# Optimization experiments

Hardware: AMD Instinct MI355X
Metric: run time of the kernel (lower is better)

Reference implementation:

```python
import jax, jax.numpy as jnp
import numpy as np

B, T, C, H, S = 4, 2048, 1024, 16, 64
LN_EPS = 1e-5
WKV_EPS = 1e-6
K_CLAMP = 30.0


def _ln(x, g, b):
    m = jnp.mean(x, axis=-1, keepdims=True)
    v = jnp.var(x, axis=-1, keepdims=True)
    return (x - m) * jax.lax.rsqrt(v + LN_EPS) * g + b


def _wkv(k, v, time_decay, time_first):
    # k, v: [B,T,H,S]; recurrence in fp32 over time
    decay = jnp.exp(-jnp.exp(time_decay.astype(jnp.float32)))  # [H,S]
    tf = jnp.exp(time_first.astype(jnp.float32))               # [H,S]
    kt = jnp.moveaxis(k, 1, 0).astype(jnp.float32)  # [T,B,H,S]
    vt = jnp.moveaxis(v, 1, 0).astype(jnp.float32)
    # t == 0 special case: state seeded with time_first factor
    w0 = jnp.exp(jnp.minimum(kt[0], K_CLAMP))
    num0 = tf * w0 * vt[0]
    den0 = tf * w0

    def step(carry, xs):
        num, den = carry
        kk, vv = xs
        w = jnp.exp(jnp.minimum(kk, K_CLAMP))
        num = decay * num + w * vv
        den = decay * den + w
        return (num, den), num / (den + WKV_EPS)

    (_, _), rest = jax.lax.scan(step, (num0, den0), (kt[1:], vt[1:]))
    out = jnp.concatenate([(num0 / (den0 + WKV_EPS))[None], rest], axis=0)  # [T,B,H,S]
    return jnp.moveaxis(out, 0, 1)  # [B,T,H,S]


def setup_inputs() -> dict:
    key = jax.random.key(0)
    ks = jax.random.split(key, 8)
    sc = 1.0 / np.sqrt(C)
    sc4 = 1.0 / np.sqrt(4 * C)
    return {
        "x": jax.random.normal(ks[0], (B, T, C), jnp.float32),
        "time_decay": jnp.full((H, S), -5.0, jnp.float32),
        "time_first": jnp.zeros((H, S), jnp.float32),
        "Wk": jax.random.normal(ks[1], (C, C), jnp.float32) * sc,
        "Wv": jax.random.normal(ks[2], (C, C), jnp.float32) * sc,
        "Wr": jax.random.normal(ks[3], (C, C), jnp.float32) * sc,
        "Wo": jax.random.normal(ks[4], (C, C), jnp.float32) * sc,
        "Wffk": jax.random.normal(ks[5], (4 * C, C), jnp.float32) * sc,
        "Wffv": jax.random.normal(ks[6], (C, 4 * C), jnp.float32) * sc4,
        "ln1_g": jnp.ones((C,), jnp.float32),
        "ln1_b": jnp.zeros((C,), jnp.float32),
        "ln2_g": jnp.ones((C,), jnp.float32),
        "ln2_b": jnp.zeros((C,), jnp.float32),
    }


def reference(x, time_decay, time_first, Wk, Wv, Wr, Wo, Wffk, Wffv, ln1_g, ln1_b, ln2_g, ln2_b):
    b, t, c = x.shape
    h, s = time_decay.shape
    xl = _ln(x, ln1_g, ln1_b)
    k = (xl @ Wk.T).reshape(b, t, h, s)
    v = (xl @ Wv.T).reshape(b, t, h, s)
    r = (xl @ Wr.T).reshape(b, t, h, s)
    wkv = _wkv(k, v, time_decay, time_first).astype(x.dtype)
    rwkv = (jax.nn.sigmoid(r) * wkv).reshape(b, t, c)
    x = x + rwkv @ Wo.T
    xl2 = _ln(x, ln2_g, ln2_b)
    ffn = (jax.nn.relu(xl2 @ Wffk.T) ** 2) @ Wffv.T
    return x + ffn
```

## Files before the change

kernel.cpp:

```cpp
#include <hip/hip_runtime.h>
#include <cstdint>
#include <cstddef>

#define TT 2048
#define CC 1024
#define HH 16
#define SS 64
#define MROWS 8192
#define KVRN 3072
#define NCH 32
#define LCH 64

using short8 = __attribute__((ext_vector_type(8))) short;
using f32x4  = __attribute__((ext_vector_type(4))) float;

__device__ __forceinline__ float b2f(unsigned short u) {
  union { unsigned int i; float f; } c; c.i = ((unsigned int)u) << 16; return c.f;
}
__device__ __forceinline__ unsigned short f2b(float f) {
  union { float f; unsigned int i; } c; c.f = f;
  unsigned int r = c.i + 0x7fffu + ((c.i >> 16) & 1u);
  return (unsigned short)(r >> 16);
}

typedef const __attribute__((address_space(1))) unsigned int* gas_ptr;
typedef __attribute__((address_space(3))) unsigned int* las_ptr;
__device__ __forceinline__ void gl_lds16(const unsigned short* g, unsigned short* l) {
  __builtin_amdgcn_global_load_lds((gas_ptr)g, (las_ptr)l, 16, 0, 0);
}

__global__ __launch_bounds__(256) void cvt_ln_kernel(const float* __restrict__ Wk,
                                                     const float* __restrict__ Wv,
                                                     const float* __restrict__ Wr,
                                                     const float* __restrict__ Wo,
                                                     const float* __restrict__ Wffk,
                                                     const float* __restrict__ Wffv,
                                                     unsigned short* __restrict__ dst,
                                                     const float* __restrict__ x,
                                                     const float* __restrict__ g,
                                                     const float* __restrict__ bta,
                                                     unsigned short* __restrict__ xlo) {
  const size_t M1 = 1048576;
  const int tid = threadIdx.x;
  if (blockIdx.x < 12288) {
    size_t i = ((size_t)blockIdx.x * 256 + tid) * 4;
    const float* src; size_t off;
    if      (i <  1 * M1) { src = Wk;   off = 0;      }
    else if (i <  2 * M1) { src = Wv;   off = 1 * M1; }
    else if (i <  3 * M1) { src = Wr;   off = 2 * M1; }
    else if (i <  4 * M1) { src = Wo;   off = 3 * M1; }
    else if (i <  8 * M1) { src = Wffk; off = 4 * M1; }
    else                  { src = Wffv; off = 8 * M1; }
    float4 v = *(const float4*)(src + (i - off));
    *(ushort4*)(dst + i) = make_ushort4(f2b(v.x), f2b(v.y), f2b(v.z), f2b(v.w));
    return;
  }
  const int row = blockIdx.x - 12288;
  const float* xr = x + (size_t)row * CC;
  float4 v = *(const float4*)(xr + tid * 4);
  float s  = v.x + v.y + v.z + v.w;
  float ss = v.x * v.x + v.y * v.y + v.z * v.z + v.w * v.w;
#pragma unroll
  for (int off = 32; off > 0; off >>= 1) {
    s  += __shfl_xor(s, off, 64);
    ss += __shfl_xor(ss, off, 64);
  }
  __shared__ float ls[4], lss[4];
  if ((tid & 63) == 0) { ls[tid >> 6] = s; lss[tid >> 6] = ss; }
  __syncthreads();
  s  = ls[0] + ls[1] + ls[2] + ls[3];
  ss = lss[0] + lss[1] + lss[2] + lss[3];
  const float mean = s * (1.0f / CC);
  const float var  = ss * (1.0f / CC) - mean * mean;
  const float rstd = rsqrtf(var + 1e-5f);
  float4 gv = *(const float4*)(g + tid * 4);
  float4 bv = *(const float4*)(bta + tid * 4);
  ushort4 o = make_ushort4(f2b((v.x - mean) * rstd * gv.x + bv.x),
                           f2b((v.y - mean) * rstd * gv.y + bv.y),
                           f2b((v.z - mean) * rstd * gv.z + bv.z),
                           f2b((v.w - mean) * rstd * gv.w + bv.w));
  *(ushort4*)(xlo + (size_t)row * CC + tid * 4) = o;
}

__global__ __launch_bounds__(256) void ln_kernel(const float* __restrict__ x,
                                                 const float* __restrict__ g,
                                                 const float* __restrict__ bta,
                                                 unsigned short* __restrict__ out,
                                                 float* __restrict__ outc) {
  const int row = blockIdx.x;
  const int tid = threadIdx.x;
  const float* xr = x + (size_t)row * CC;
  float4 v = *(const float4*)(xr + tid * 4);
  *(float4*)(outc + (size_t)row * CC + tid * 4) = v;
  float s  = v.x + v.y + v.z + v.w;
  float ss = v.x * v.x + v.y * v.y + v.z * v.z + v.w * v.w;
#pragma unroll
  for (int off = 32; off > 0; off >>= 1) {
    s  += __shfl_xor(s, off, 64);
    ss += __shfl_xor(ss, off, 64);
  }
  __shared__ float ls[4], lss[4];
  if ((tid & 63) == 0) { ls[tid >> 6] = s; lss[tid >> 6] = ss; }
  __syncthreads();
  s  = ls[0] + ls[1] + ls[2] + ls[3];
  ss = lss[0] + lss[1] + lss[2] + lss[3];
  const float mean = s * (1.0f / CC);
  const float var  = ss * (1.0f / CC) - mean * mean;
  const float rstd = rsqrtf(var + 1e-5f);
  float4 gv = *(const float4*)(g + tid * 4);
  float4 bv = *(const float4*)(bta + tid * 4);
  ushort4 o = make_ushort4(f2b((v.x - mean) * rstd * gv.x + bv.x),
                           f2b((v.y - mean) * rstd * gv.y + bv.y),
                           f2b((v.z - mean) * rstd * gv.z + bv.z),
                           f2b((v.w - mean) * rstd * gv.w + bv.w));
  *(ushort4*)(out + (size_t)row * CC + tid * 4) = o;
}

__global__ __launch_bounds__(64) void wkv_local(const unsigned short* __restrict__ kvr,
                                                const float* __restrict__ td,
                                                const float* __restrict__ tfp,
                                                float* __restrict__ scratch) {
  const int blk = blockIdx.x;
  const int bh = blk >> 5, c = blk & (NCH - 1);
  const int b = bh >> 4, h = bh & 15;
  const int s = threadIdx.x;
  const int ch = h * SS + s;
  const float e = __expf(td[ch]);
  const float d = __expf(-e);
  const float tfir = __expf(tfp[ch]);
  size_t idx = ((size_t)b * TT + (size_t)c * LCH) * KVRN + ch;
  float num = 0.f, den = 0.f;
  for (int i = 0; i < LCH; ++i) {
    float w = __expf(fminf(b2f(kvr[idx]), 30.f));
    if (c == 0 && i == 0) w *= tfir;
    float vv = b2f(kvr[idx + 1024]);
    num = d * num + w * vv;
    den = d * den + w;
    idx += KVRN;
  }
  float* o = scratch + ((size_t)bh * NCH + c) * 128;
  o[s] = num; o[64 + s] = den;
}

__global__ __launch_bounds__(64) void wkv_emit(const unsigned short* __restrict__ kvr,
                                               const float* __restrict__ td,
                                               const float* __restrict__ tfp,
                                               const float* __restrict__ scratch,
                                               unsigned short* __restrict__ rwkv) {
  const int blk = blockIdx.x;
  const int bh = blk >> 5, c = blk & (NCH - 1);
  const int b = bh >> 4, h = bh & 15;
  const int s = threadIdx.x;
  const int ch = h * SS + s;
  const float e = __expf(td[ch]);
  const float d = __expf(-e);
  const float Dc = __expf(-e * (float)LCH);
  const float tfir = __expf(tfp[ch]);
  float num = 0.f, den = 0.f;
  const float* sc = scratch + (size_t)bh * NCH * 128;
  for (int cc = 0; cc < c; ++cc) {
    num = Dc * num + sc[cc * 128 + s];
    den = Dc * den + sc[cc * 128 + 64 + s];
  }
  size_t idx = ((size_t)b * TT + (size_t)c * LCH) * KVRN + ch;
  size_t odx = ((size_t)b * TT + (size_t)c * LCH) * CC + ch;
  for (int i = 0; i < LCH; ++i) {
    float w = __expf(fminf(b2f(kvr[idx]), 30.f));
    if (c == 0 && i == 0) w *= tfir;
    float vv = b2f(kvr[idx + 1024]);
    num = d * num + w * vv;
    den = d * den + w;
    float o = num / (den + 1e-6f);
    float rr = b2f(kvr[idx + 2048]);
    float sg = 1.0f / (1.0f + __expf(-rr));
    rwkv[odx] = f2b(sg * o);
    idx += KVRN;
    odx += CC;
  }
}

#define GBAR do { __builtin_amdgcn_sched_barrier(0); __builtin_amdgcn_s_barrier(); \
                  __builtin_amdgcn_sched_barrier(0); } while (0)
#define WAIT_LGKM0 do { __builtin_amdgcn_s_waitcnt(0xC07F); \
                        __builtin_amdgcn_sched_barrier(0); } while (0)
#define WAIT_VM8   do { __builtin_amdgcn_sched_barrier(0); \
                        __builtin_amdgcn_s_waitcnt(0x0F78); \
                        __builtin_amdgcn_sched_barrier(0); } while (0)

template <int EP>
__global__ __launch_bounds__(512, 2) void gemm256(const unsigned short* __restrict__ A,
                                                  const unsigned short* __restrict__ Bw,
                                                  void* __restrict__ outv,
                                                  const float* __restrict__ res,
                                                  int N, int Kfull, int Kloop) {
  __shared__ __align__(16) unsigned short As[2][2][256][32];
  __shared__ __align__(16) unsigned short Bs[2][2][256][32];
  const int tid = threadIdx.x;

  const int nbn = N >> 8;
  const int per_grp = nbn << 4;
  const int bid = blockIdx.x;
  const int grp = bid / per_grp;
  const int rem = bid - grp * per_grp;
  const int bm = (grp << 4) + (rem & 15);
  const int bn = rem >> 4;
  const int koffb = blockIdx.y * Kloop;
  const int nt = Kloop >> 6;

  const int r0  = tid >> 2;
  const int qsl = ((tid & 3) ^ (r0 & 3)) << 3;
  const unsigned short* gA0 = A  + (size_t)(bm * 256 + r0) * Kfull + koffb + qsl;
  const unsigned short* gA1 = gA0 + (size_t)128 * Kfull;
  const unsigned short* gB0 = Bw + (size_t)(bn * 256 + r0) * Kfull + koffb + qsl;
  const unsigned short* gB1 = gB0 + (size_t)128 * Kfull;
  const int ldsoff = tid * 8;

  auto stA = [&](int bb, int kk, int ko) {
    unsigned short* d = &As[bb][kk][0][0];
    gl_lds16(gA0 + ko, d + ldsoff);
    gl_lds16(gA1 + ko, d + ldsoff + 4096);
  };
  auto stB = [&](int bb, int kk, int ko) {
    unsigned short* d = &Bs[bb][kk][0][0];
    gl_lds16(gB0 + ko, d + ldsoff);
    gl_lds16(gB1 + ko, d + ldsoff + 4096);
  };

  const int lane = tid & 63, w = tid >> 6;
  const int wr = w >> 2, wn = w & 3;
  const int r16 = lane & 15, q = lane >> 4;
  const int qx = (q ^ (r16 & 3)) << 3;
  const unsigned short* fA = &As[0][0][0][0] + (wr * 128 + r16) * 32 + qx;
  const unsigned short* fB = &Bs[0][0][0][0] + (wn * 64  + r16) * 32 + qx;

  f32x4 acc[8][4] = {};
  short8 af[4], bf_[4];

  stA(0, 0, 0);  stB(0, 0, 0);
  stA(0, 1, 32); stB(0, 1, 32);
  stA(1, 0, 64); stB(1, 0, 64);
  WAIT_VM8;
  GBAR;

  int b = 0;
  for (int t = 0; t < nt; ++t, b ^= 1) {
    const unsigned short* fAb = fA + b * 16384;
    const unsigned short* fBb = fB + b * 16384;
    const int t1 = (t + 1 < nt) ? t + 1 : nt - 1;
    const int t2 = (t + 2 < nt) ? t + 2 : nt - 1;
    const int ko1 = (t1 << 6) + 32;
    const int ko2 = (t2 << 6);

#pragma unroll
    for (int i = 0; i < 4; ++i) af[i]  = *(const short8*)(fAb + i * 512);
#pragma unroll
    for (int i = 0; i < 4; ++i) bf_[i] = *(const short8*)(fBb + i * 512);
    stA(b ^ 1, 1, ko1);
    GBAR;
    WAIT_LGKM0;
    __builtin_amdgcn_s_setprio(1);
#pragma unroll
    for (int mi = 0; mi < 4; ++mi)
#pragma unroll
      for (int ni = 0; ni < 4; ++ni)
        acc[mi][ni] = __builtin_amdgcn_mfma_f32_16x16x32_bf16(af[mi], bf_[ni], acc[mi][ni], 0, 0, 0);
    __builtin_amdgcn_s_setprio(0);
    GBAR;

#pragma unroll
    for (int i = 0; i < 4; ++i) af[i] = *(const short8*)(fAb + (4 + i) * 512);
    stB(b ^ 1, 1, ko1);
    WAIT_VM8;
    GBAR;
    WAIT_LGKM0;
    __builtin_amdgcn_s_setprio(1);
#pragma unroll
    for (int mi = 0; mi < 4; ++mi)
#pragma unroll
      for (int ni = 0; ni < 4; ++ni)
        acc[4 + mi][ni] = __builtin_amdgcn_mfma_f32_16x16x32_bf16(af[mi], bf_[ni], acc[4 + mi][ni], 0, 0, 0);
    __builtin_amdgcn_s_setprio(0);
    GBAR;

#pragma unroll
    for (int i = 0; i < 4; ++i) af[i]  = *(const short8*)(fAb + 8192 + i * 512);
#pragma unroll
    for (int i = 0; i < 4; ++i) bf_[i] = *(const short8*)(fBb + 8192 + i * 512);
    stA(b, 0, ko2);
    GBAR;
    WAIT_LGKM0;
    __builtin_amdgcn_s_setprio(1);
#pragma unroll
    for (int mi = 0; mi < 4; ++mi)
#pragma unroll
      for (int ni = 0; ni < 4; ++ni)
        acc[mi][ni] = __builtin_amdgcn_mfma_f32_16x16x32_bf16(af[mi], bf_[ni], acc[mi][ni], 0, 0, 0);
    __builtin_amdgcn_s_setprio(0);
    GBAR;

#pragma unroll
    for (int i = 0; i < 4; ++i) af[i] = *(const short8*)(fAb + 8192 + (4 + i) * 512);
    stB(b, 0, ko2);
    WAIT_VM8;
    GBAR;
    WAIT_LGKM0;
    __builtin_amdgcn_s_setprio(1);
#pragma unroll
    for (int mi = 0; mi < 4; ++mi)
#pragma unroll
      for (int ni = 0; ni < 4; ++ni)
        acc[4 + mi][ni] = __builtin_amdgcn_mfma_f32_16x16x32_bf16(af[mi], bf_[ni], acc[4 + mi][ni], 0, 0, 0);
    __builtin_amdgcn_s_setprio(0);
    GBAR;
  }

  __builtin_amdgcn_s_waitcnt(0x0070);

#pragma unroll
  for (int mi = 0; mi < 8; ++mi) {
#pragma unroll
    for (int r = 0; r < 4; ++r) {
      const int grow = bm * 256 + wr * 128 + mi * 16 + q * 4 + r;
#pragma unroll
      for (int ni = 0; ni < 4; ++ni) {
        const int gcol = bn * 256 + wn * 64 + ni * 16 + r16;
        const size_t idx = (size_t)grow * N + gcol;
        float vv = acc[mi][ni][r];
        if (EP == 2) {
          ((float*)outv)[idx] = res[idx] + vv;
        } else if (EP == 3) {
          unsafeAtomicAdd((float*)outv + idx, vv);
        } else {
          if (EP == 1) { vv = fmaxf(vv, 0.0f); vv = vv * vv; }
          ((unsigned short*)outv)[idx] = f2b(vv);
        }
      }
    }
  }
}

extern "C" void kernel_launch(void* const* d_in, const int* in_sizes, int n_in,
                              void* d_out, int out_size, void* d_ws, size_t ws_size,
                              hipStream_t stream) {
  const float* x    = (const float*)d_in[0];
  const float* td   = (const float*)d_in[1];
  const float* tf   = (const float*)d_in[2];
  const float* Wk   = (const float*)d_in[3];
  const float* Wv   = (const float*)d_in[4];
  const float* Wr   = (const float*)d_in[5];
  const float* Wo   = (const float*)d_in[6];
  const float* Wffk = (const float*)d_in[7];
  const float* Wffv = (const float*)d_in[8];
  const float* g1   = (const float*)d_in[9];
  const float* b1   = (const float*)d_in[10];
  const float* g2   = (const float*)d_in[11];
  const float* b2   = (const float*)d_in[12];
  float* out = (float*)d_out;

  char* ws = (char*)d_ws;
  const size_t MB = 1024ull * 1024ull;
  unsigned short* WB    = (unsigned short*)ws;
  unsigned short* WkvrB = WB;
  unsigned short* WoB   = WB + 3 * 1048576;
  unsigned short* WfkB  = WB + 4 * 1048576;
  unsigned short* WfvB  = WB + 8 * 1048576;
  unsigned short* xl    = (unsigned short*)(ws + 24 * MB);
  unsigned short* kvr   = (unsigned short*)(ws + 40 * MB);
  float*          x2    = (float*)(ws + 88 * MB);
  unsigned short* hb    = (unsigned short*)(ws + 120 * MB);
  float*          wkvS  = (float*)(ws + 184 * MB);
  unsigned short* rwkv  = xl;
  unsigned short* xl2   = kvr;

  cvt_ln_kernel<<<12288 + MROWS, 256, 0, stream>>>(Wk, Wv, Wr, Wo, Wffk, Wffv, WB,
                                                   x, g1, b1, xl);

  gemm256<0><<<dim3((KVRN / 256) * (MROWS / 256), 1), 512, 0, stream>>>(
      xl, WkvrB, kvr, nullptr, KVRN, 1024, 1024);

  wkv_local<<<64 * NCH, 64, 0, stream>>>(kvr, td, tf, wkvS);
  wkv_emit<<<64 * NCH, 64, 0, stream>>>(kvr, td, tf, wkvS, rwkv);

  gemm256<2><<<dim3((CC / 256) * (MROWS / 256), 1), 512, 0, stream>>>(
      rwkv, WoB, x2, x, CC, 1024, 1024);

  ln_kernel<<<MROWS, 256, 0, stream>>>(x2, g2, b2, xl2, out);

  gemm256<1><<<dim3((4096 / 256) * (MROWS / 256), 1), 512, 0, stream>>>(
      xl2, WfkB, hb, nullptr, 4096, 1024, 1024);

  gemm256<3><<<dim3((CC / 256) * (MROWS / 256), 2), 512, 0, stream>>>(
      hb, WfvB, out, nullptr, CC, 4096, 2048);
}
```

Baseline: 485.2 us.

## Restructure GEMM into 4-stage single-barrier pipeline and split-K the output projection

```diff
diff --git a/kernel.cpp b/kernel.cpp
--- a/kernel.cpp
+++ b/kernel.cpp
@@ -39,7 +39,8 @@
                                                      const float* __restrict__ x,
                                                      const float* __restrict__ g,
                                                      const float* __restrict__ bta,
-                                                     unsigned short* __restrict__ xlo) {
+                                                     unsigned short* __restrict__ xlo,
+                                                     float* __restrict__ x2o) {
   const size_t M1 = 1048576;
   const int tid = threadIdx.x;
   if (blockIdx.x < 12288) {
@@ -58,6 +59,7 @@
   const int row = blockIdx.x - 12288;
   const float* xr = x + (size_t)row * CC;
   float4 v = *(const float4*)(xr + tid * 4);
+  *(float4*)(x2o + (size_t)row * CC + tid * 4) = v;
   float s  = v.x + v.y + v.z + v.w;
   float ss = v.x * v.x + v.y * v.y + v.z * v.z + v.w * v.w;
 #pragma unroll
@@ -179,7 +181,7 @@
   }
 }
 
-#define GBAR do { __builtin_amdgcn_sched_barrier(0); __builtin_amdgcn_s_barrier(); \
+#define GBAR do { __builtin_amdgcn_sched_barrier(0); asm volatile("s_barrier"); \
                   __builtin_amdgcn_sched_barrier(0); } while (0)
 #define WAIT_LGKM0 do { __builtin_amdgcn_s_waitcnt(0xC07F); \
                         __builtin_amdgcn_sched_barrier(0); } while (0)
@@ -193,8 +195,8 @@
                                                   void* __restrict__ outv,
                                                   const float* __restrict__ res,
                                                   int N, int Kfull, int Kloop) {
-  __shared__ __align__(16) unsigned short As[2][2][256][32];
-  __shared__ __align__(16) unsigned short Bs[2][2][256][32];
+  __shared__ __align__(16) unsigned short As[4][256][32];
+  __shared__ __align__(16) unsigned short Bs[4][256][32];
   const int tid = threadIdx.x;
 
   const int nbn = N >> 8;
@@ -205,113 +207,61 @@
   const int bm = (grp << 4) + (rem & 15);
   const int bn = rem >> 4;
   const int koffb = blockIdx.y * Kloop;
-  const int nt = Kloop >> 6;
+  const int nt = Kloop >> 5;
 
   const int r0  = tid >> 2;
-  const int qsl = ((tid & 3) ^ (r0 & 3)) << 3;
+  const int qsl = ((tid & 3) ^ ((tid >> 3) & 3)) << 3;
   const unsigned short* gA0 = A  + (size_t)(bm * 256 + r0) * Kfull + koffb + qsl;
   const unsigned short* gA1 = gA0 + (size_t)128 * Kfull;
   const unsigned short* gB0 = Bw + (size_t)(bn * 256 + r0) * Kfull + koffb + qsl;
   const unsigned short* gB1 = gB0 + (size_t)128 * Kfull;
   const int ldsoff = tid * 8;
 
-  auto stA = [&](int bb, int kk, int ko) {
-    unsigned short* d = &As[bb][kk][0][0];
-    gl_lds16(gA0 + ko, d + ldsoff);
-    gl_lds16(gA1 + ko, d + ldsoff + 4096);
-  };
-  auto stB = [&](int bb, int kk, int ko) {
-    unsigned short* d = &Bs[bb][kk][0][0];
-    gl_lds16(gB0 + ko, d + ldsoff);
-    gl_lds16(gB1 + ko, d + ldsoff + 4096);
+  auto stage = [&](int bb, int ko) {
+    unsigned short* da = &As[bb][0][0];
+    unsigned short* db = &Bs[bb][0][0];
+    gl_lds16(gA0 + ko, da + ldsoff);
+    gl_lds16(gA1 + ko, da + ldsoff + 4096);
+    gl_lds16(gB0 + ko, db + ldsoff);
+    gl_lds16(gB1 + ko, db + ldsoff + 4096);
   };
 
   const int lane = tid & 63, w = tid >> 6;
   const int wr = w >> 2, wn = w & 3;
   const int r16 = lane & 15, q = lane >> 4;
-  const int qx = (q ^ (r16 & 3)) << 3;
-  const unsigned short* fA = &As[0][0][0][0] + (wr * 128 + r16) * 32 + qx;
-  const unsigned short* fB = &Bs[0][0][0][0] + (wn * 64  + r16) * 32 + qx;
+  const int qx = (q ^ ((r16 >> 1) & 3)) << 3;
+  const unsigned short* fA = &As[0][0][0] + (wr * 128 + r16) * 32 + qx;
+  const unsigned short* fB = &Bs[0][0][0] + (wn * 64  + r16) * 32 + qx;
 
   f32x4 acc[8][4] = {};
-  short8 af[4], bf_[4];
-
-  stA(0, 0, 0);  stB(0, 0, 0);
-  stA(0, 1, 32); stB(0, 1, 32);
-  stA(1, 0, 64); stB(1, 0, 64);
+  short8 af[8], bf_[4];
+
+  stage(0, 0);
+  stage(1, 32);
+  stage(2, 64);
   WAIT_VM8;
   GBAR;
-
-  int b = 0;
-  for (int t = 0; t < nt; ++t, b ^= 1) {
-    const unsigned short* fAb = fA + b * 16384;
-    const unsigned short* fBb = fB + b * 16384;
-    const int t1 = (t + 1 < nt) ? t + 1 : nt - 1;
-    const int t2 = (t + 2 < nt) ? t + 2 : nt - 1;
-    const int ko1 = (t1 << 6) + 32;
-    const int ko2 = (t2 << 6);
-
-#pragma unroll
-    for (int i = 0; i < 4; ++i) af[i]  = *(const short8*)(fAb + i * 512);
+  WAIT_LGKM0;
+
+  for (int t = 0; t < nt; ++t) {
+    const unsigned short* fAb = fA + (t & 3) * 8192;
+    const unsigned short* fBb = fB + (t & 3) * 8192;
+#pragma unroll
+    for (int i = 0; i < 8; ++i) af[i]  = *(const short8*)(fAb + i * 512);
 #pragma unroll
     for (int i = 0; i < 4; ++i) bf_[i] = *(const short8*)(fBb + i * 512);
-    stA(b ^ 1, 1, ko1);
-    GBAR;
-    WAIT_LGKM0;
-    __builtin_amdgcn_s_setprio(1);
-#pragma unroll
-    for (int mi = 0; mi < 4; ++mi)
-#pragma unroll
-      for (int ni = 0; ni < 4; ++ni)
-        acc[mi][ni] = __builtin_amdgcn_mfma_f32_16x16x32_bf16(af[mi], bf_[ni], acc[mi][ni], 0, 0, 0);
-    __builtin_amdgcn_s_setprio(0);
-    GBAR;
-
-#pragma unroll
-    for (int i = 0; i < 4; ++i) af[i] = *(const short8*)(fAb + (4 + i) * 512);
-    stB(b ^ 1, 1, ko1);
+    const int t3 = (t + 3 < nt) ? t + 3 : nt - 1;
+    stage((t + 3) & 3, t3 << 5);
     WAIT_VM8;
     GBAR;
     WAIT_LGKM0;
     __builtin_amdgcn_s_setprio(1);
 #pragma unroll
-    for (int mi = 0; mi < 4; ++mi)
-#pragma unroll
-      for (int ni = 0; ni < 4; ++ni)
-        acc[4 + mi][ni] = __builtin_amdgcn_mfma_f32_16x16x32_bf16(af[mi], bf_[ni], acc[4 + mi][ni], 0, 0, 0);
-    __builtin_amdgcn_s_setprio(0);
-    GBAR;
-
-#pragma unroll
-    for (int i = 0; i < 4; ++i) af[i]  = *(const short8*)(fAb + 8192 + i * 512);
-#pragma unroll
-    for (int i = 0; i < 4; ++i) bf_[i] = *(const short8*)(fBb + 8192 + i * 512);
-    stA(b, 0, ko2);
-    GBAR;
-    WAIT_LGKM0;
-    __builtin_amdgcn_s_setprio(1);
-#pragma unroll
-    for (int mi = 0; mi < 4; ++mi)
+    for (int mi = 0; mi < 8; ++mi)
 #pragma unroll
       for (int ni = 0; ni < 4; ++ni)
         acc[mi][ni] = __builtin_amdgcn_mfma_f32_16x16x32_bf16(af[mi], bf_[ni], acc[mi][ni], 0, 0, 0);
     __builtin_amdgcn_s_setprio(0);
-    GBAR;
-
-#pragma unroll
-    for (int i = 0; i < 4; ++i) af[i] = *(const short8*)(fAb + 8192 + (4 + i) * 512);
-    stB(b, 0, ko2);
-    WAIT_VM8;
-    GBAR;
-    WAIT_LGKM0;
-    __builtin_amdgcn_s_setprio(1);
-#pragma unroll
-    for (int mi = 0; mi < 4; ++mi)
-#pragma unroll
-      for (int ni = 0; ni < 4; ++ni)
-        acc[4 + mi][ni] = __builtin_amdgcn_mfma_f32_16x16x32_bf16(af[mi], bf_[ni], acc[4 + mi][ni], 0, 0, 0);
-    __builtin_amdgcn_s_setprio(0);
-    GBAR;
   }
 
   __builtin_amdgcn_s_waitcnt(0x0070);
@@ -373,7 +323,7 @@
   unsigned short* xl2   = kvr;
 
   cvt_ln_kernel<<<12288 + MROWS, 256, 0, stream>>>(Wk, Wv, Wr, Wo, Wffk, Wffv, WB,
-                                                   x, g1, b1, xl);
+                                                   x, g1, b1, xl, x2);
 
   gemm256<0><<<dim3((KVRN / 256) * (MROWS / 256), 1), 512, 0, stream>>>(
       xl, WkvrB, kvr, nullptr, KVRN, 1024, 1024);
@@ -381,8 +331,8 @@
   wkv_local<<<64 * NCH, 64, 0, stream>>>(kvr, td, tf, wkvS);
   wkv_emit<<<64 * NCH, 64, 0, stream>>>(kvr, td, tf, wkvS, rwkv);
 
-  gemm256<2><<<dim3((CC / 256) * (MROWS / 256), 1), 512, 0, stream>>>(
-      rwkv, WoB, x2, x, CC, 1024, 1024);
+  gemm256<3><<<dim3((CC / 256) * (MROWS / 256), 2), 512, 0, stream>>>(
+      rwkv, WoB, x2, nullptr, CC, 1024, 512);
 
   ln_kernel<<<MROWS, 256, 0, stream>>>(x2, g2, b2, xl2, out);
 
```

After: 484.8 us. Within noise of the previous version (-0.1%).
